# Optimization experiments

Measured on AMD Instinct MI355X. Metric: run time of the kernel, lower is better.

## Reference

```python
import jax, jax.numpy as jnp
import numpy as np

B, C, V = 1024, 512, 256  # batch, num_conjunctions, num_variables


def setup_inputs() -> dict:
    key = jax.random.key(0)
    k1, k2, k3 = jax.random.split(key, 3)
    x0 = jax.random.uniform(k1, (B, V), dtype=jnp.float32)
    # torch init: conj = 1 - 2*rand  -> uniform in (-1, 1)
    conjunctions = 1.0 - 2.0 * jax.random.uniform(k2, (C, 2 * V), dtype=jnp.float32)
    # rw = 10 - 20*rand -> uniform in (-10, 10)
    rule_weights = 10.0 - 20.0 * jax.random.uniform(k3, (C,), dtype=jnp.float32)
    return {"x0": x0, "conjunctions": conjunctions, "rule_weights": rule_weights}


def reference(x0, conjunctions, rule_weights):
    mu = jax.nn.sigmoid(conjunctions)            # (C, 2V)
    x = jnp.concatenate((x0, 1.0 - x0), axis=1)  # (B, 2V)
    # fuzzy-AND: broadcast mul-add then min over literal axis
    x_pot = mu[None, :, :] * x[:, None, :] + (1.0 - mu)[None, :, :]  # (B, C, 2V)
    fit = jnp.min(x_pot, axis=-1)                # (B, C)
    return 5.0 + jnp.sum(rule_weights * fit, axis=-1)  # (B,)
```

## Files before the change

kernel.cpp:

```cpp
#include <hip/hip_runtime.h>


#define B_    1024
#define C_    512
#define V_    256
#define TWOV  512

#define CPW    64
#define NCHUNK (C_ / CPW)
#define BPB    8
#define NBG    (B_ / BPB)
#define WAVES  8
#define VPW    32
#define HVP    8

__global__ __launch_bounds__(256) void k_prep(const float* __restrict__ conj,
                                              float2* __restrict__ muT2) {
    const int c = blockIdx.x;
    const int v = threadIdx.x;
    float z1 = conj[(size_t)c * TWOV + v];
    float z2 = conj[(size_t)c * TWOV + V_ + v];
    float m1 = 1.0f / (1.0f + __expf(-z1));
    float m2 = 1.0f / (1.0f + __expf(-z2));
    muT2[(size_t)(v >> 1) * (2 * C_) + c * 2 + (v & 1)] = make_float2(m1, m2);
}

__global__ __launch_bounds__(512, 6) void k_main(const float* __restrict__ x0,
                                                 const float4* __restrict__ muT4,
                                                 const float* __restrict__ rw,
                                                 float* __restrict__ partial) {
    const int tid   = threadIdx.x;
    const int lane  = tid & 63;
    const int wave  = tid >> 6;
    const int chunk = blockIdx.y;
    const int c     = chunk * CPW + lane;
    const int bg    = blockIdx.x;
    const int v0    = wave * VPW;

    __shared__ float4 xs[BPB * V_ / 4];
    __shared__ float  red[BPB * WAVES * 64];

    {
        const float4* xg = reinterpret_cast<const float4*>(x0 + (size_t)bg * BPB * V_);
        xs[tid] = xg[tid];
    }

    const float4* mup = muT4 + (size_t)(v0 >> 1) * C_ + c;

    float m[BPB];
#pragma unroll
    for (int i = 0; i < BPB; ++i) m[i] = 0.0f;

    __syncthreads();

#pragma unroll
    for (int h = 0; h < 2; ++h) {
        float4 mr[HVP];
#pragma unroll
        for (int p = 0; p < HVP; ++p)
            mr[p] = mup[(size_t)(h * HVP + p) * C_];
#pragma unroll
        for (int p = 0; p < HVP; ++p)
            asm volatile("" : "+v"(mr[p].x), "+v"(mr[p].y), "+v"(mr[p].z), "+v"(mr[p].w));

#pragma unroll
        for (int bi = 0; bi < BPB; ++bi) {
            const int xb = bi * (V_ / 4) + (v0 >> 2) + h * 4;
            float4 xa = xs[xb + 0];
            float4 xc = xs[xb + 1];
            float4 xd = xs[xb + 2];
            float4 xe = xs[xb + 3];
            float mm = m[bi];
#define STEP(P, XA, XB) \
            mm = fmaxf(mm, fmaxf(__builtin_fmaf(-mr[P].x, (XA), mr[P].x), mr[P].y * (XA))); \
            mm = fmaxf(mm, fmaxf(__builtin_fmaf(-mr[P].z, (XB), mr[P].z), mr[P].w * (XB)));
            STEP(0, xa.x, xa.y)  STEP(1, xa.z, xa.w)
            STEP(2, xc.x, xc.y)  STEP(3, xc.z, xc.w)
            STEP(4, xd.x, xd.y)  STEP(5, xd.z, xd.w)
            STEP(6, xe.x, xe.y)  STEP(7, xe.z, xe.w)
#undef STEP
            m[bi] = mm;
        }
    }

#pragma unroll
    for (int bi = 0; bi < BPB; ++bi)
        red[bi * (WAVES * 64) + tid] = m[bi];
    __syncthreads();

    float mm = red[wave * (WAVES * 64) + lane];
#pragma unroll
    for (int k = 1; k < WAVES; ++k)
        mm = fmaxf(mm, red[wave * (WAVES * 64) + k * 64 + lane]);
    float s = rw[c] * (1.0f - mm);
    s += __shfl_xor(s, 1, 64);
    s += __shfl_xor(s, 2, 64);
    s += __shfl_xor(s, 4, 64);
    s += __shfl_xor(s, 8, 64);
    s += __shfl_xor(s, 16, 64);
    s += __shfl_xor(s, 32, 64);
    if (lane == 0)
        partial[(size_t)chunk * B_ + bg * BPB + wave] = s;
}

__global__ __launch_bounds__(256) void k_final(const float* __restrict__ partial,
                                               float* __restrict__ out) {
    int b = blockIdx.x * 256 + threadIdx.x;
    if (b < B_) {
        float s = 5.0f;
#pragma unroll
        for (int k = 0; k < NCHUNK; ++k) s += partial[(size_t)k * B_ + b];
        out[b] = s;
    }
}

__global__ __launch_bounds__(256) void k_naive(const float* __restrict__ x0,
                                               const float* __restrict__ conj,
                                               const float* __restrict__ rw,
                                               float* __restrict__ out) {
    int b = blockIdx.x;
    int t = threadIdx.x;
    __shared__ float red[256];
    float acc = 0.0f;
    for (int c = t; c < C_; c += 256) {
        float m = 0.0f;
        for (int v = 0; v < V_; ++v) {
            float mu1 = 1.0f / (1.0f + expf(-conj[(size_t)c * TWOV + v]));
            float mu2 = 1.0f / (1.0f + expf(-conj[(size_t)c * TWOV + V_ + v]));
            float x = x0[(size_t)b * V_ + v];
            m = fmaxf(m, fmaxf(mu1 * (1.0f - x), mu2 * x));
        }
        acc += rw[c] * (1.0f - m);
    }
    red[t] = acc;
    __syncthreads();
    for (int s = 128; s > 0; s >>= 1) {
        if (t < s) red[t] += red[t + s];
        __syncthreads();
    }
    if (t == 0) out[b] = 5.0f + red[0];
}

extern "C" void kernel_launch(void* const* d_in, const int* in_sizes, int n_in,
                              void* d_out, int out_size, void* d_ws, size_t ws_size,
                              hipStream_t stream) {
    const float* x0   = (const float*)d_in[0];
    const float* conj = (const float*)d_in[1];
    const float* rw   = (const float*)d_in[2];
    float* out = (float*)d_out;

    const size_t mu_floats  = (size_t)(V_ / 2) * C_ * 4;
    const size_t part_elems = (size_t)NCHUNK * B_;
    const size_t need = (mu_floats + part_elems) * sizeof(float);

    if (ws_size < need) {
        k_naive<<<B_, 256, 0, stream>>>(x0, conj, rw, out);
        return;
    }

    float4* muT4   = (float4*)d_ws;
    float* partial = (float*)d_ws + mu_floats;

    k_prep<<<C_, 256, 0, stream>>>(conj, (float2*)muT4);
    dim3 grid(NBG, NCHUNK);
    k_main<<<grid, 512, 0, stream>>>(x0, muT4, rw, partial);
    k_final<<<(B_ + 255) / 256, 256, 0, stream>>>(partial, out);
}
```

Measured before the change: 25.06 us.

## Process two conjunction groups per thread to reuse LDS x loads

Each thread now handles two conjunctions (lane and lane+64), doubling the conjunctions per block and halving the number of chunks. Each x value read from shared memory is reused across twice as many mu registers, cutting LDS traffic per unit of compute and halving the x staging and partial-sum writes. The cost is doubled register use for mu and the accumulators, with the occupancy hint lowered from 6 to 4 blocks, and fewer total blocks in the grid.

```diff
diff --git a/kernel.cpp b/kernel.cpp
--- a/kernel.cpp
+++ b/kernel.cpp
@@ -6,7 +6,7 @@
 #define V_    256
 #define TWOV  512
 
-#define CPW    64
+#define CPW    128
 #define NCHUNK (C_ / CPW)
 #define BPB    8
 #define NBG    (B_ / BPB)
@@ -25,7 +25,7 @@
     muT2[(size_t)(v >> 1) * (2 * C_) + c * 2 + (v & 1)] = make_float2(m1, m2);
 }
 
-__global__ __launch_bounds__(512, 6) void k_main(const float* __restrict__ x0,
+__global__ __launch_bounds__(512, 4) void k_main(const float* __restrict__ x0,
                                                  const float4* __restrict__ muT4,
                                                  const float* __restrict__ rw,
                                                  float* __restrict__ partial) {
@@ -33,35 +33,40 @@
     const int lane  = tid & 63;
     const int wave  = tid >> 6;
     const int chunk = blockIdx.y;
-    const int c     = chunk * CPW + lane;
+    const int cA    = chunk * CPW + lane;
+    const int cB    = cA + 64;
     const int bg    = blockIdx.x;
     const int v0    = wave * VPW;
 
     __shared__ float4 xs[BPB * V_ / 4];
-    __shared__ float  red[BPB * WAVES * 64];
+    __shared__ float  red[2 * BPB * WAVES * 64];
 
     {
         const float4* xg = reinterpret_cast<const float4*>(x0 + (size_t)bg * BPB * V_);
         xs[tid] = xg[tid];
     }
 
-    const float4* mup = muT4 + (size_t)(v0 >> 1) * C_ + c;
+    const float4* mup = muT4 + (size_t)(v0 >> 1) * C_ + cA;
 
-    float m[BPB];
+    float mA[BPB], mB[BPB];
 #pragma unroll
-    for (int i = 0; i < BPB; ++i) m[i] = 0.0f;
+    for (int i = 0; i < BPB; ++i) { mA[i] = 0.0f; mB[i] = 0.0f; }
 
     __syncthreads();
 
 #pragma unroll
     for (int h = 0; h < 2; ++h) {
-        float4 mr[HVP];
+        float4 mrA[HVP], mrB[HVP];
 #pragma unroll
-        for (int p = 0; p < HVP; ++p)
-            mr[p] = mup[(size_t)(h * HVP + p) * C_];
+        for (int p = 0; p < HVP; ++p) {
+            mrA[p] = mup[(size_t)(h * HVP + p) * C_];
+            mrB[p] = mup[(size_t)(h * HVP + p) * C_ + 64];
+        }
 #pragma unroll
-        for (int p = 0; p < HVP; ++p)
-            asm volatile("" : "+v"(mr[p].x), "+v"(mr[p].y), "+v"(mr[p].z), "+v"(mr[p].w));
+        for (int p = 0; p < HVP; ++p) {
+            asm volatile("" : "+v"(mrA[p].x), "+v"(mrA[p].y), "+v"(mrA[p].z), "+v"(mrA[p].w));
+            asm volatile("" : "+v"(mrB[p].x), "+v"(mrB[p].y), "+v"(mrB[p].z), "+v"(mrB[p].w));
+        }
 
 #pragma unroll
         for (int bi = 0; bi < BPB; ++bi) {
@@ -70,29 +75,36 @@
             float4 xc = xs[xb + 1];
             float4 xd = xs[xb + 2];
             float4 xe = xs[xb + 3];
-            float mm = m[bi];
+            float ma = mA[bi], mb = mB[bi];
 #define STEP(P, XA, XB) \
-            mm = fmaxf(mm, fmaxf(__builtin_fmaf(-mr[P].x, (XA), mr[P].x), mr[P].y * (XA))); \
-            mm = fmaxf(mm, fmaxf(__builtin_fmaf(-mr[P].z, (XB), mr[P].z), mr[P].w * (XB)));
+            ma = fmaxf(ma, fmaxf(__builtin_fmaf(-mrA[P].x, (XA), mrA[P].x), mrA[P].y * (XA))); \
+            ma = fmaxf(ma, fmaxf(__builtin_fmaf(-mrA[P].z, (XB), mrA[P].z), mrA[P].w * (XB))); \
+            mb = fmaxf(mb, fmaxf(__builtin_fmaf(-mrB[P].x, (XA), mrB[P].x), mrB[P].y * (XA))); \
+            mb = fmaxf(mb, fmaxf(__builtin_fmaf(-mrB[P].z, (XB), mrB[P].z), mrB[P].w * (XB)));
             STEP(0, xa.x, xa.y)  STEP(1, xa.z, xa.w)
             STEP(2, xc.x, xc.y)  STEP(3, xc.z, xc.w)
             STEP(4, xd.x, xd.y)  STEP(5, xd.z, xd.w)
             STEP(6, xe.x, xe.y)  STEP(7, xe.z, xe.w)
 #undef STEP
-            m[bi] = mm;
+            mA[bi] = ma; mB[bi] = mb;
         }
     }
 
 #pragma unroll
-    for (int bi = 0; bi < BPB; ++bi)
-        red[bi * (WAVES * 64) + tid] = m[bi];
+    for (int bi = 0; bi < BPB; ++bi) {
+        red[bi * (WAVES * 64) + tid] = mA[bi];
+        red[(BPB + bi) * (WAVES * 64) + tid] = mB[bi];
+    }
     __syncthreads();
 
-    float mm = red[wave * (WAVES * 64) + lane];
+    float ma = red[wave * (WAVES * 64) + lane];
+    float mb = red[(BPB + wave) * (WAVES * 64) + lane];
 #pragma unroll
-    for (int k = 1; k < WAVES; ++k)
-        mm = fmaxf(mm, red[wave * (WAVES * 64) + k * 64 + lane]);
-    float s = rw[c] * (1.0f - mm);
+    for (int k = 1; k < WAVES; ++k) {
+        ma = fmaxf(ma, red[wave * (WAVES * 64) + k * 64 + lane]);
+        mb = fmaxf(mb, red[(BPB + wave) * (WAVES * 64) + k * 64 + lane]);
+    }
+    float s = rw[cA] * (1.0f - ma) + rw[cB] * (1.0f - mb);
     s += __shfl_xor(s, 1, 64);
     s += __shfl_xor(s, 2, 64);
     s += __shfl_xor(s, 4, 64);
```

After: 25.06 us. About the same (-0.0%).

## Double batch rows per block and replace final reduction kernel with atomics

Applied to the files above, without the earlier changes.

Each block now processes 16 batch rows instead of 8, so each loaded mu value is reused across more rows, and occupancy hints drop from 6 to 4. The separate final-sum kernel is removed: the prep kernel initialises the output to 5.0 and the main kernel atomically adds each chunk's partial sum into the output. This saves one kernel launch and the partial-buffer round trip, at the cost of more registers per thread, fewer resident waves, and a nondeterministic summation order.

```diff
diff --git a/kernel.cpp b/kernel.cpp
--- a/kernel.cpp
+++ b/kernel.cpp
@@ -8,16 +8,18 @@
 
 #define CPW    64
 #define NCHUNK (C_ / CPW)
-#define BPB    8
+#define BPB    16
 #define NBG    (B_ / BPB)
 #define WAVES  8
 #define VPW    32
 #define HVP    8
 
 __global__ __launch_bounds__(256) void k_prep(const float* __restrict__ conj,
-                                              float2* __restrict__ muT2) {
+                                              float2* __restrict__ muT2,
+                                              float* __restrict__ out) {
     const int c = blockIdx.x;
     const int v = threadIdx.x;
+    if (c < 4) out[c * 256 + v] = 5.0f;
     float z1 = conj[(size_t)c * TWOV + v];
     float z2 = conj[(size_t)c * TWOV + V_ + v];
     float m1 = 1.0f / (1.0f + __expf(-z1));
@@ -25,10 +27,10 @@
     muT2[(size_t)(v >> 1) * (2 * C_) + c * 2 + (v & 1)] = make_float2(m1, m2);
 }
 
-__global__ __launch_bounds__(512, 6) void k_main(const float* __restrict__ x0,
+__global__ __launch_bounds__(512, 4) void k_main(const float* __restrict__ x0,
                                                  const float4* __restrict__ muT4,
                                                  const float* __restrict__ rw,
-                                                 float* __restrict__ partial) {
+                                                 float* __restrict__ out) {
     const int tid   = threadIdx.x;
     const int lane  = tid & 63;
     const int wave  = tid >> 6;
@@ -42,7 +44,8 @@
 
     {
         const float4* xg = reinterpret_cast<const float4*>(x0 + (size_t)bg * BPB * V_);
-        xs[tid] = xg[tid];
+        xs[tid]       = xg[tid];
+        xs[tid + 512] = xg[tid + 512];
     }
 
     const float4* mup = muT4 + (size_t)(v0 >> 1) * C_ + c;
@@ -88,29 +91,24 @@
         red[bi * (WAVES * 64) + tid] = m[bi];
     __syncthreads();
 
-    float mm = red[wave * (WAVES * 64) + lane];
+    const float rwc = rw[c];
+    float m0 = red[wave * (WAVES * 64) + lane];
+    float m1 = red[(wave + 8) * (WAVES * 64) + lane];
 #pragma unroll
-    for (int k = 1; k < WAVES; ++k)
-        mm = fmaxf(mm, red[wave * (WAVES * 64) + k * 64 + lane]);
-    float s = rw[c] * (1.0f - mm);
-    s += __shfl_xor(s, 1, 64);
-    s += __shfl_xor(s, 2, 64);
-    s += __shfl_xor(s, 4, 64);
-    s += __shfl_xor(s, 8, 64);
-    s += __shfl_xor(s, 16, 64);
-    s += __shfl_xor(s, 32, 64);
-    if (lane == 0)
-        partial[(size_t)chunk * B_ + bg * BPB + wave] = s;
-}
-
-__global__ __launch_bounds__(256) void k_final(const float* __restrict__ partial,
-                                               float* __restrict__ out) {
-    int b = blockIdx.x * 256 + threadIdx.x;
-    if (b < B_) {
-        float s = 5.0f;
+    for (int k = 1; k < WAVES; ++k) {
+        m0 = fmaxf(m0, red[wave * (WAVES * 64) + k * 64 + lane]);
+        m1 = fmaxf(m1, red[(wave + 8) * (WAVES * 64) + k * 64 + lane]);
+    }
+    float s0 = rwc * (1.0f - m0);
+    float s1 = rwc * (1.0f - m1);
 #pragma unroll
-        for (int k = 0; k < NCHUNK; ++k) s += partial[(size_t)k * B_ + b];
-        out[b] = s;
+    for (int d = 1; d < 64; d <<= 1) {
+        s0 += __shfl_xor(s0, d, 64);
+        s1 += __shfl_xor(s1, d, 64);
+    }
+    if (lane == 0) {
+        atomicAdd(&out[bg * BPB + wave], s0);
+        atomicAdd(&out[bg * BPB + wave + 8], s1);
     }
 }
 
@@ -149,20 +147,17 @@
     const float* rw   = (const float*)d_in[2];
     float* out = (float*)d_out;
 
-    const size_t mu_floats  = (size_t)(V_ / 2) * C_ * 4;
-    const size_t part_elems = (size_t)NCHUNK * B_;
-    const size_t need = (mu_floats + part_elems) * sizeof(float);
+    const size_t mu_floats = (size_t)(V_ / 2) * C_ * 4;
+    const size_t need = mu_floats * sizeof(float);
 
     if (ws_size < need) {
         k_naive<<<B_, 256, 0, stream>>>(x0, conj, rw, out);
         return;
     }
 
-    float4* muT4   = (float4*)d_ws;
-    float* partial = (float*)d_ws + mu_floats;
+    float4* muT4 = (float4*)d_ws;
 
-    k_prep<<<C_, 256, 0, stream>>>(conj, (float2*)muT4);
+    k_prep<<<C_, 256, 0, stream>>>(conj, (float2*)muT4, out);
     dim3 grid(NBG, NCHUNK);
-    k_main<<<grid, 512, 0, stream>>>(x0, muT4, rw, partial);
-    k_final<<<(B_ + 255) / 256, 256, 0, stream>>>(partial, out);
+    k_main<<<grid, 512, 0, stream>>>(x0, muT4, rw, out);
 }
```

After: 24.89 us. About the same (-0.7%).
